# Kernel tuning notes

Measured on AMD Instinct MI355X. Metric: run time of the kernel, lower is better.

Reference implementation:

```python
import jax, jax.numpy as jnp
import numpy as np
from functools import partial

THRESH = 0.6      # objectness sigmoid threshold (forward arg `thresh`)
CASE = 416.0      # input image size (forward arg `case`)
NMS_THRESH = 0.7  # nms(boxes, 0.7, mode='inter')
K_PER_SCALE = 512 # fixed candidate cap per scale (jit-safe stand-in for nonzero())
NEG = -1e9


def _decode_scale(out, t, anchors):
    """out: [N, 3*(5+nc), H, W] -> (boxes [K,9], valid [K]) top-K by objectness."""
    N, C, H, W = out.shape
    v = out.transpose(0, 2, 3, 1).reshape(N, H, W, 3, -1)  # [N,H,W,3,5+nc]
    f = v.dtype
    obj = jax.nn.sigmoid(v[..., 0])                        # cfd = sigmoid(vecs[:,0])
    gy = jnp.arange(H, dtype=f).reshape(1, H, 1, 1)        # idxs[:,1] (row)
    gx = jnp.arange(W, dtype=f).reshape(1, 1, W, 1)        # idxs[:,2] (col)
    gn = jnp.arange(N, dtype=f).reshape(N, 1, 1, 1)
    cx = (gx + v[..., 1]) * t / CASE
    cy = (gy + v[..., 2]) * t / CASE
    w = anchors[:, 0] * jnp.exp(v[..., 3]) / CASE          # anchors[a,0], a = last axis
    h = anchors[:, 1] * jnp.exp(v[..., 4]) / CASE
    cls = jnp.argmax(v[..., 5:], axis=-1).astype(f)
    parts = jnp.broadcast_arrays(gn, cx, cy, w, h, obj, cls, gy + 0 * cx, gx + 0 * cx)
    boxes = jnp.stack(parts, axis=-1).reshape(-1, 9)       # [N*H*W*3, 9]
    mask = (obj > THRESH).reshape(-1)
    score = jnp.where(mask, obj.reshape(-1), NEG)
    k = min(K_PER_SCALE, score.shape[0])
    top_s, top_i = jax.lax.top_k(score, k)
    boxes_k = jnp.take(boxes, top_i, axis=0)
    valid_k = top_s > NEG / 2
    if k < K_PER_SCALE:  # pad to fixed K
        pad = K_PER_SCALE - k
        boxes_k = jnp.concatenate([boxes_k, jnp.zeros((pad, 9), f)], 0)
        valid_k = jnp.concatenate([valid_k, jnp.zeros((pad,), bool)], 0)
    return boxes_k, valid_k


def _nms_inter(boxes, valid):
    """Greedy NMS, iou mode 'inter' = inter_area / min(area_i, area_j)."""
    score = jnp.where(valid, boxes[:, 5], NEG)
    order = jnp.argsort(-score)
    boxes = jnp.take(boxes, order, axis=0)
    valid = jnp.take(valid, order)
    cx, cy, w, h = boxes[:, 1], boxes[:, 2], boxes[:, 3], boxes[:, 4]
    x1, y1, x2, y2 = cx - w / 2, cy - h / 2, cx + w / 2, cy + h / 2
    area = jnp.maximum(x2 - x1, 0) * jnp.maximum(y2 - y1, 0)
    ix = jnp.maximum(0.0, jnp.minimum(x2[:, None], x2[None]) - jnp.maximum(x1[:, None], x1[None]))
    iy = jnp.maximum(0.0, jnp.minimum(y2[:, None], y2[None]) - jnp.maximum(y1[:, None], y1[None]))
    inter = ix * iy
    iou = inter / jnp.maximum(jnp.minimum(area[:, None], area[None]), 1e-9)
    M = boxes.shape[0]
    idx = jnp.arange(M)

    def body(i, keep):
        sup = (iou[i] > NMS_THRESH) & keep[i] & (idx > i)
        return keep & ~sup

    keep = jax.lax.fori_loop(0, M, body, valid)
    return boxes * keep[:, None].astype(boxes.dtype)  # suppressed rows zeroed


def reference(out13, out26, out52, anchors13, anchors26, anchors52):
    b13, v13 = _decode_scale(out13, 32.0, anchors13)
    b26, v26 = _decode_scale(out26, 16.0, anchors26)
    b52, v52 = _decode_scale(out52, 8.0, anchors52)
    boxes = jnp.concatenate([b13, b26, b52], axis=0)   # [3K, 9]
    valid = jnp.concatenate([v13, v26, v52], axis=0)
    return _nms_inter(boxes, valid)


def setup_inputs() -> dict:
    key = jax.random.key(0)
    k = jax.random.split(key, 6)
    N, NC = 32, 80
    C = 3 * (5 + NC)
    return {
        "out13": jax.random.normal(k[0], (N, C, 13, 13), jnp.float32),
        "out26": jax.random.normal(k[1], (N, C, 26, 26), jnp.float32),
        "out52": jax.random.normal(k[2], (N, C, 52, 52), jnp.float32),
        "anchors13": jnp.array([[116, 90], [156, 198], [373, 326]], jnp.float32),
        "anchors26": jnp.array([[30, 61], [62, 45], [59, 119]], jnp.float32),
        "anchors52": jnp.array([[10, 13], [16, 30], [33, 23]], jnp.float32),
    }
```

## Files before the change

kernel.cpp:

```cpp
#include <hip/hip_runtime.h>
#include <stdint.h>

#define KPS 512
#define NBOX 1536
#define NBINS 1024
#define CAP 96

#define S13 16224
#define S26 64896
#define S52 259584
#define TOTCELL 340704

__device__ __forceinline__ uint32_t f2u(float x){ union{float f;uint32_t u;}v; v.f=x; return v.u; }
__device__ __forceinline__ float u2f(uint32_t x){ union{float f;uint32_t u;}v; v.u=x; return v.f; }

__device__ __forceinline__ int binOf(float s){
    int b = (int)((s - 0.6f) * 2560.0f);
    if (b < 0) b = 0;
    if (b > NBINS-1) b = NBINS-1;
    return b;
}

__global__ void k_init(int* hist){
    int id = blockIdx.x*256 + threadIdx.x;
    if (id < 3*NBINS) hist[id] = 0;
}

__global__ void k_score(const float* __restrict__ o13, const float* __restrict__ o26,
                        const float* __restrict__ o52,
                        unsigned long long* __restrict__ bucket, int* __restrict__ hist){
    int id = blockIdx.x*256 + threadIdx.x;
    if (id >= TOTCELL) return;
    int scale, idl, H;
    const float* src;
    if (id < S13)            { scale=0; idl=id;            H=13; src=o13; }
    else if (id < S13+S26)   { scale=1; idl=id-S13;        H=26; src=o26; }
    else                     { scale=2; idl=id-(S13+S26);  H=52; src=o52; }
    int HW = H*H;
    int p  = idl / HW;
    int hw = idl - p*HW;
    int n  = p / 3;
    int a  = p - n*3;
    float x = src[(size_t)(n*255 + a*85)*HW + hw];
    float s = (float)(1.0 / (1.0 + exp(-(double)x)));
    if (s > 0.6f){
        int cidx = (n*HW + hw)*3 + a;
        unsigned long long key = ((unsigned long long)f2u(s) << 20)
            | ((unsigned long long)(2-scale) << 18)
            | (unsigned long long)(262143 - cidx);
        int slot = scale*NBINS + binOf(s);
        int pos = atomicAdd(&hist[slot], 1);
        if (pos < CAP) bucket[(size_t)slot*CAP + pos] = key;
    }
}

__global__ void __launch_bounds__(1024) k_selfin(const int* __restrict__ hist,
                        const unsigned long long* __restrict__ bucket,
                        unsigned long long* __restrict__ sel, int* __restrict__ cnt){
    int s = blockIdx.x, t = threadIdx.x;
    __shared__ int suf[NBINS];
    __shared__ unsigned long long un[640];
    __shared__ int sB;
    int h = hist[s*NBINS + t];
    suf[t] = h; __syncthreads();
    for (int d = 1; d < NBINS; d <<= 1){
        int v = (t + d < NBINS) ? suf[t + d] : 0;
        __syncthreads();
        suf[t] += v;
        __syncthreads();
    }
    int total = suf[0];
    int A = (t < NBINS-1) ? suf[t+1] : 0;
    if (t == 0 && total < KPS) sB = -1;
    if (A < KPS && A + h >= KPS) sB = t;
    __syncthreads();
    int B = sB;
    int Bg = (B < 0) ? 0 : B;
    if (t + Bg < NBINS){
        int b = Bg + t;
        int cb = hist[s*NBINS + b]; if (cb > CAP) cb = CAP;
        int off = (b == NBINS-1) ? 0 : suf[b+1];
        for (int e = 0; e < cb; e++)
            un[off + e] = bucket[(size_t)(s*NBINS + b)*CAP + e];
    }
    __syncthreads();
    int hB = hist[s*NBINS + Bg]; if (hB > CAP) hB = CAP;
    int E = ((Bg == NBINS-1) ? 0 : suf[Bg+1]) + hB;
    int Nsel = (E < KPS) ? E : KPS;
    for (int e = t; e < E; e += 1024){
        unsigned long long k = un[e];
        int rank = 0;
        for (int q = 0; q < E; q++) rank += (un[q] > k) ? 1 : 0;
        if (rank < Nsel) sel[s*KPS + rank] = k;
    }
    if (t < KPS && t >= Nsel) sel[s*KPS + t] = 0ull;
    if (t == 0) cnt[s] = Nsel;
}

__global__ void k_decode_merge(const float* __restrict__ o13, const float* __restrict__ o26,
                         const float* __restrict__ o52,
                         const float* __restrict__ a13, const float* __restrict__ a26,
                         const float* __restrict__ a52,
                         const unsigned long long* __restrict__ sel, const int* __restrict__ cnt,
                         float* __restrict__ sboxes, unsigned long long* __restrict__ vwords){
    __shared__ unsigned long long sk[NBOX];
    int t = threadIdx.x;
    for (int r = t; r < NBOX; r += 256) sk[r] = sel[r];
    __syncthreads();
    int wv = t >> 6, lane = t & 63;
    int b = blockIdx.x*4 + wv;
    unsigned long long key = sk[b];
    int pc = 0;
    for (int q = lane; q < NBOX; q += 64){
        unsigned long long kq = sk[q];
        pc += (kq > key || (kq == key && q < b)) ? 1 : 0;
    }
    #pragma unroll
    for (int off = 32; off; off >>= 1) pc += __shfl_xor(pc, off);
    int rank = pc;
    float* row = sboxes + rank*12;
    if ((key >> 20) == 0ull){
        if (lane < 9) row[lane] = 0.f;
    } else {
        int scale = 2 - (int)((key >> 18) & 3ull);
        int cidx  = 262143 - (int)(key & 0x3FFFFull);
        uint32_t sbits = (uint32_t)(key >> 20);
        const float* src; const float* anch; int H; float tt;
        if (scale == 0){ src=o13; anch=a13; H=13; tt=32.f; }
        else if (scale == 1){ src=o26; anch=a26; H=26; tt=16.f; }
        else { src=o52; anch=a52; H=52; tt=8.f; }
        int HW = H*H;
        int a  = cidx % 3;
        int hw = (cidx/3) % HW;
        int n  = cidx / (3*HW);
        int hh = hw / H;
        int ww = hw - hh*H;
        const float* cellbase = src + (size_t)(n*255 + a*85)*HW + hw;
        float bv = cellbase[(size_t)(5 + lane)*HW];
        int bi = lane;
        if (lane < 16){
            float v2 = cellbase[(size_t)(69 + lane)*HW];
            if (v2 > bv){ bv = v2; bi = 64 + lane; }
        }
        #pragma unroll
        for (int off=32; off; off>>=1){
            float vo = __shfl_xor(bv, off);
            int io = __shfl_xor(bi, off);
            if (vo > bv || (vo == bv && io < bi)){ bv = vo; bi = io; }
        }
        if (lane == 0){
            float v1 = cellbase[(size_t)1*HW];
            float v2 = cellbase[(size_t)2*HW];
            float v3 = cellbase[(size_t)3*HW];
            float v4 = cellbase[(size_t)4*HW];
            float cx = ((float)ww + v1) * tt / 416.0f;
            float cy = ((float)hh + v2) * tt / 416.0f;
            float e3 = (float)exp((double)v3);
            float e4 = (float)exp((double)v4);
            float bw = anch[a*2+0] * e3 / 416.0f;
            float bh = anch[a*2+1] * e4 / 416.0f;
            row[0] = (float)n;  row[1] = cx; row[2] = cy; row[3] = bw; row[4] = bh;
            row[5] = u2f(sbits); row[6] = (float)bi; row[7] = (float)hh; row[8] = (float)ww;
        }
    }
    if (blockIdx.x == 0 && t < 24){
        int nv = cnt[0] + cnt[1] + cnt[2];
        int rem = nv - t*64;
        vwords[t] = rem >= 64 ? ~0ull : (rem <= 0 ? 0ull : ((1ull << rem) - 1ull));
    }
}

__global__ void k_masks(const float* __restrict__ sboxes, unsigned* __restrict__ Tcol,
                        unsigned long long* __restrict__ diagR){
    int i = blockIdx.x;
    int lane = threadIdx.x;
    int gi = i >> 6;
    float cxi = sboxes[i*12+1], cyi = sboxes[i*12+2], wi = sboxes[i*12+3], hi = sboxes[i*12+4];
    float x1i = cxi - wi/2.0f, y1i = cyi - hi/2.0f, x2i = cxi + wi/2.0f, y2i = cyi + hi/2.0f;
    float ari = fmaxf(x2i-x1i, 0.f) * fmaxf(y2i-y1i, 0.f);
    unsigned colbits = 0u;
    for (int c=0; c<24; c++){
        int j = c*64 + lane;
        float cxj = sboxes[j*12+1], cyj = sboxes[j*12+2], wj = sboxes[j*12+3], hj = sboxes[j*12+4];
        float x1j = cxj - wj/2.0f, y1j = cyj - hj/2.0f, x2j = cxj + wj/2.0f, y2j = cyj + hj/2.0f;
        float arj = fmaxf(x2j-x1j, 0.f) * fmaxf(y2j-y1j, 0.f);
        float ix = fmaxf(0.f, fminf(x2i, x2j) - fmaxf(x1i, x1j));
        float iy = fmaxf(0.f, fminf(y2i, y2j) - fmaxf(y1i, y1j));
        float inter = ix * iy;
        float iou = inter / fmaxf(fminf(ari, arj), 1e-9f);
        bool sb = (iou > 0.7f) && (j > i);
        colbits |= sb ? (1u << c) : 0u;
    }
    Tcol[(size_t)i*64 + lane] = colbits;
    unsigned long long rowbits = __ballot(((colbits >> gi) & 1u) != 0u);
    if (lane == 0) diagR[i] = rowbits;
}

__device__ __forceinline__ unsigned long long readlane64(unsigned long long v, int i){
    unsigned lo = (unsigned)__builtin_amdgcn_readlane((int)(unsigned)v, i);
    unsigned hi = (unsigned)__builtin_amdgcn_readlane((int)(unsigned)(v >> 32), i);
    return ((unsigned long long)hi << 32) | (unsigned long long)lo;
}

__global__ void k_nms_out(const float* __restrict__ sboxes, const unsigned long long* __restrict__ vwords,
                          const unsigned long long* __restrict__ diagR, const unsigned* __restrict__ Tcol,
                          float* __restrict__ out){
    __shared__ unsigned long long keepw[24];
    __shared__ unsigned partial[2][4][64];
    int t = threadIdx.x;
    int wv = t >> 6, lane = t & 63;
    unsigned SS = 0u;
    unsigned long long rowR = diagR[lane];
    unsigned long long vcur = vwords[0];
    unsigned rows[16];
    {
        const unsigned* b0 = Tcol + (size_t)(wv*16)*64 + lane;
        #pragma unroll
        for (int i=0;i<16;i++) rows[i] = b0[i*64];
    }
    for (int g = 0; g < 24; g++){
        unsigned long long Rnext = (g < 23) ? diagR[(g+1)*64 + lane] : 0ull;
        unsigned long long vnext = (g < 23) ? vwords[g+1] : 0ull;
        bool live = (((vcur >> lane) & 1ull) != 0ull) && (((SS >> g) & 1u) == 0u);
        unsigned long long pend = __ballot(live);
        unsigned long long Z = __ballot(live && ((rowR & pend) != 0ull));
        unsigned long long kept = pend;
        unsigned long long iter = Z;
        while (iter){
            int i = __ffsll((long long)iter) - 1;
            iter &= iter - 1ull;
            if ((kept >> i) & 1ull){
                unsigned long long sup = readlane64(rowR, i);
                kept &= ~sup;
                iter &= ~sup;
            }
        }
        if (t == 0) keepw[g] = kept;
        unsigned kbits = (unsigned)((kept >> (wv*16)) & 0xFFFFull);
        unsigned acc = 0u;
        #pragma unroll
        for (int i=0;i<16;i++) acc |= (0u - ((kbits >> i) & 1u)) & rows[i];
        if (g < 23){
            const unsigned* nb = Tcol + (size_t)((g+1)*64 + wv*16)*64 + lane;
            #pragma unroll
            for (int i=0;i<16;i++) rows[i] = nb[i*64];
        }
        partial[g & 1][wv][lane] = acc;
        __syncthreads();
        SS |= partial[g & 1][0][lane] | partial[g & 1][1][lane]
            | partial[g & 1][2][lane] | partial[g & 1][3][lane];
        rowR = Rnext; vcur = vnext;
    }
    for (int e=t; e<NBOX*9; e+=256){
        int r = e / 9;
        int c = e - r*9;
        bool kp = ((keepw[r >> 6] >> (r & 63)) & 1ull) != 0ull;
        out[e] = kp ? sboxes[r*12 + c] : 0.f;
    }
}

extern "C" void kernel_launch(void* const* d_in, const int* in_sizes, int n_in,
                              void* d_out, int out_size, void* d_ws, size_t ws_size,
                              hipStream_t stream){
    const float* o13 = (const float*)d_in[0];
    const float* o26 = (const float*)d_in[1];
    const float* o52 = (const float*)d_in[2];
    const float* a13 = (const float*)d_in[3];
    const float* a26 = (const float*)d_in[4];
    const float* a52 = (const float*)d_in[5];
    char* ws = (char*)d_ws;
    unsigned long long* bucket = (unsigned long long*)(ws);
    unsigned* Tcol            = (unsigned*)(ws);
    int* hist                 = (int*)(ws + 2359296);
    int* cnt                  = (int*)(ws + 2371584);
    unsigned long long* sel   = (unsigned long long*)(ws + 2371712);
    float* sboxes             = (float*)(ws + 2384000);
    unsigned long long* vw    = (unsigned long long*)(ws + 2457728);
    unsigned long long* diagR = (unsigned long long*)(ws + 2457984);
    float* out = (float*)d_out;

    k_init        <<<12, 256, 0, stream>>>(hist);
    k_score       <<<(TOTCELL + 255)/256, 256, 0, stream>>>(o13, o26, o52, bucket, hist);
    k_selfin      <<<3, 1024, 0, stream>>>(hist, bucket, sel, cnt);
    k_decode_merge<<<NBOX/4, 256, 0, stream>>>(o13, o26, o52, a13, a26, a52, sel, cnt, sboxes, vw);
    k_masks       <<<NBOX, 64, 0, stream>>>(sboxes, Tcol, diagR);
    k_nms_out     <<<1, 256, 0, stream>>>(sboxes, vw, diagR, Tcol, out);
}
```

Baseline: 230.8 us.

## Fuse all six stages into one cooperative kernel with grid-wide syncs

Replaces the six separate launches (init, score, select, decode/merge, masks, NMS) with one persistent cooperative kernel of 256 blocks × 1024 threads. Stages are separated by grid.sync() barriers, and per-stage shared memory is overlaid in a union. The aim is to remove per-launch overhead and the idle gaps between small dependent kernels. In exchange, several stages now run on fewer, larger blocks: mask building uses 96 blocks instead of 1536, and scoring uses a grid-stride loop. Each grid barrier also has its own cost.

New measurement: 355.5 us. 1.54x slower.

```diff
diff --git a/kernel.cpp b/kernel.cpp
--- a/kernel.cpp
+++ b/kernel.cpp
@@ -1,5 +1,8 @@
 #include <hip/hip_runtime.h>
+#include <hip/hip_cooperative_groups.h>
 #include <stdint.h>
+
+namespace cg = cooperative_groups;
 
 #define KPS 512
 #define NBOX 1536
@@ -21,241 +24,253 @@
     return b;
 }
 
-__global__ void k_init(int* hist){
-    int id = blockIdx.x*256 + threadIdx.x;
-    if (id < 3*NBINS) hist[id] = 0;
-}
-
-__global__ void k_score(const float* __restrict__ o13, const float* __restrict__ o26,
-                        const float* __restrict__ o52,
-                        unsigned long long* __restrict__ bucket, int* __restrict__ hist){
-    int id = blockIdx.x*256 + threadIdx.x;
-    if (id >= TOTCELL) return;
-    int scale, idl, H;
-    const float* src;
-    if (id < S13)            { scale=0; idl=id;            H=13; src=o13; }
-    else if (id < S13+S26)   { scale=1; idl=id-S13;        H=26; src=o26; }
-    else                     { scale=2; idl=id-(S13+S26);  H=52; src=o52; }
-    int HW = H*H;
-    int p  = idl / HW;
-    int hw = idl - p*HW;
-    int n  = p / 3;
-    int a  = p - n*3;
-    float x = src[(size_t)(n*255 + a*85)*HW + hw];
-    float s = (float)(1.0 / (1.0 + exp(-(double)x)));
-    if (s > 0.6f){
-        int cidx = (n*HW + hw)*3 + a;
-        unsigned long long key = ((unsigned long long)f2u(s) << 20)
-            | ((unsigned long long)(2-scale) << 18)
-            | (unsigned long long)(262143 - cidx);
-        int slot = scale*NBINS + binOf(s);
-        int pos = atomicAdd(&hist[slot], 1);
-        if (pos < CAP) bucket[(size_t)slot*CAP + pos] = key;
-    }
-}
-
-__global__ void __launch_bounds__(1024) k_selfin(const int* __restrict__ hist,
-                        const unsigned long long* __restrict__ bucket,
-                        unsigned long long* __restrict__ sel, int* __restrict__ cnt){
-    int s = blockIdx.x, t = threadIdx.x;
-    __shared__ int suf[NBINS];
-    __shared__ unsigned long long un[640];
-    __shared__ int sB;
-    int h = hist[s*NBINS + t];
-    suf[t] = h; __syncthreads();
-    for (int d = 1; d < NBINS; d <<= 1){
-        int v = (t + d < NBINS) ? suf[t + d] : 0;
-        __syncthreads();
-        suf[t] += v;
-        __syncthreads();
-    }
-    int total = suf[0];
-    int A = (t < NBINS-1) ? suf[t+1] : 0;
-    if (t == 0 && total < KPS) sB = -1;
-    if (A < KPS && A + h >= KPS) sB = t;
-    __syncthreads();
-    int B = sB;
-    int Bg = (B < 0) ? 0 : B;
-    if (t + Bg < NBINS){
-        int b = Bg + t;
-        int cb = hist[s*NBINS + b]; if (cb > CAP) cb = CAP;
-        int off = (b == NBINS-1) ? 0 : suf[b+1];
-        for (int e = 0; e < cb; e++)
-            un[off + e] = bucket[(size_t)(s*NBINS + b)*CAP + e];
-    }
-    __syncthreads();
-    int hB = hist[s*NBINS + Bg]; if (hB > CAP) hB = CAP;
-    int E = ((Bg == NBINS-1) ? 0 : suf[Bg+1]) + hB;
-    int Nsel = (E < KPS) ? E : KPS;
-    for (int e = t; e < E; e += 1024){
-        unsigned long long k = un[e];
-        int rank = 0;
-        for (int q = 0; q < E; q++) rank += (un[q] > k) ? 1 : 0;
-        if (rank < Nsel) sel[s*KPS + rank] = k;
-    }
-    if (t < KPS && t >= Nsel) sel[s*KPS + t] = 0ull;
-    if (t == 0) cnt[s] = Nsel;
-}
-
-__global__ void k_decode_merge(const float* __restrict__ o13, const float* __restrict__ o26,
-                         const float* __restrict__ o52,
-                         const float* __restrict__ a13, const float* __restrict__ a26,
-                         const float* __restrict__ a52,
-                         const unsigned long long* __restrict__ sel, const int* __restrict__ cnt,
-                         float* __restrict__ sboxes, unsigned long long* __restrict__ vwords){
-    __shared__ unsigned long long sk[NBOX];
-    int t = threadIdx.x;
-    for (int r = t; r < NBOX; r += 256) sk[r] = sel[r];
-    __syncthreads();
-    int wv = t >> 6, lane = t & 63;
-    int b = blockIdx.x*4 + wv;
-    unsigned long long key = sk[b];
-    int pc = 0;
-    for (int q = lane; q < NBOX; q += 64){
-        unsigned long long kq = sk[q];
-        pc += (kq > key || (kq == key && q < b)) ? 1 : 0;
-    }
-    #pragma unroll
-    for (int off = 32; off; off >>= 1) pc += __shfl_xor(pc, off);
-    int rank = pc;
-    float* row = sboxes + rank*12;
-    if ((key >> 20) == 0ull){
-        if (lane < 9) row[lane] = 0.f;
-    } else {
-        int scale = 2 - (int)((key >> 18) & 3ull);
-        int cidx  = 262143 - (int)(key & 0x3FFFFull);
-        uint32_t sbits = (uint32_t)(key >> 20);
-        const float* src; const float* anch; int H; float tt;
-        if (scale == 0){ src=o13; anch=a13; H=13; tt=32.f; }
-        else if (scale == 1){ src=o26; anch=a26; H=26; tt=16.f; }
-        else { src=o52; anch=a52; H=52; tt=8.f; }
-        int HW = H*H;
-        int a  = cidx % 3;
-        int hw = (cidx/3) % HW;
-        int n  = cidx / (3*HW);
-        int hh = hw / H;
-        int ww = hw - hh*H;
-        const float* cellbase = src + (size_t)(n*255 + a*85)*HW + hw;
-        float bv = cellbase[(size_t)(5 + lane)*HW];
-        int bi = lane;
-        if (lane < 16){
-            float v2 = cellbase[(size_t)(69 + lane)*HW];
-            if (v2 > bv){ bv = v2; bi = 64 + lane; }
-        }
-        #pragma unroll
-        for (int off=32; off; off>>=1){
-            float vo = __shfl_xor(bv, off);
-            int io = __shfl_xor(bi, off);
-            if (vo > bv || (vo == bv && io < bi)){ bv = vo; bi = io; }
-        }
-        if (lane == 0){
-            float v1 = cellbase[(size_t)1*HW];
-            float v2 = cellbase[(size_t)2*HW];
-            float v3 = cellbase[(size_t)3*HW];
-            float v4 = cellbase[(size_t)4*HW];
-            float cx = ((float)ww + v1) * tt / 416.0f;
-            float cy = ((float)hh + v2) * tt / 416.0f;
-            float e3 = (float)exp((double)v3);
-            float e4 = (float)exp((double)v4);
-            float bw = anch[a*2+0] * e3 / 416.0f;
-            float bh = anch[a*2+1] * e4 / 416.0f;
-            row[0] = (float)n;  row[1] = cx; row[2] = cy; row[3] = bw; row[4] = bh;
-            row[5] = u2f(sbits); row[6] = (float)bi; row[7] = (float)hh; row[8] = (float)ww;
-        }
-    }
-    if (blockIdx.x == 0 && t < 24){
-        int nv = cnt[0] + cnt[1] + cnt[2];
-        int rem = nv - t*64;
-        vwords[t] = rem >= 64 ? ~0ull : (rem <= 0 ? 0ull : ((1ull << rem) - 1ull));
-    }
-}
-
-__global__ void k_masks(const float* __restrict__ sboxes, unsigned* __restrict__ Tcol,
-                        unsigned long long* __restrict__ diagR){
-    int i = blockIdx.x;
-    int lane = threadIdx.x;
-    int gi = i >> 6;
-    float cxi = sboxes[i*12+1], cyi = sboxes[i*12+2], wi = sboxes[i*12+3], hi = sboxes[i*12+4];
-    float x1i = cxi - wi/2.0f, y1i = cyi - hi/2.0f, x2i = cxi + wi/2.0f, y2i = cyi + hi/2.0f;
-    float ari = fmaxf(x2i-x1i, 0.f) * fmaxf(y2i-y1i, 0.f);
-    unsigned colbits = 0u;
-    for (int c=0; c<24; c++){
-        int j = c*64 + lane;
-        float cxj = sboxes[j*12+1], cyj = sboxes[j*12+2], wj = sboxes[j*12+3], hj = sboxes[j*12+4];
-        float x1j = cxj - wj/2.0f, y1j = cyj - hj/2.0f, x2j = cxj + wj/2.0f, y2j = cyj + hj/2.0f;
-        float arj = fmaxf(x2j-x1j, 0.f) * fmaxf(y2j-y1j, 0.f);
-        float ix = fmaxf(0.f, fminf(x2i, x2j) - fmaxf(x1i, x1j));
-        float iy = fmaxf(0.f, fminf(y2i, y2j) - fmaxf(y1i, y1j));
-        float inter = ix * iy;
-        float iou = inter / fmaxf(fminf(ari, arj), 1e-9f);
-        bool sb = (iou > 0.7f) && (j > i);
-        colbits |= sb ? (1u << c) : 0u;
-    }
-    Tcol[(size_t)i*64 + lane] = colbits;
-    unsigned long long rowbits = __ballot(((colbits >> gi) & 1u) != 0u);
-    if (lane == 0) diagR[i] = rowbits;
-}
-
 __device__ __forceinline__ unsigned long long readlane64(unsigned long long v, int i){
     unsigned lo = (unsigned)__builtin_amdgcn_readlane((int)(unsigned)v, i);
     unsigned hi = (unsigned)__builtin_amdgcn_readlane((int)(unsigned)(v >> 32), i);
     return ((unsigned long long)hi << 32) | (unsigned long long)lo;
 }
 
-__global__ void k_nms_out(const float* __restrict__ sboxes, const unsigned long long* __restrict__ vwords,
-                          const unsigned long long* __restrict__ diagR, const unsigned* __restrict__ Tcol,
-                          float* __restrict__ out){
-    __shared__ unsigned long long keepw[24];
-    __shared__ unsigned partial[2][4][64];
-    int t = threadIdx.x;
-    int wv = t >> 6, lane = t & 63;
-    unsigned SS = 0u;
-    unsigned long long rowR = diagR[lane];
-    unsigned long long vcur = vwords[0];
-    unsigned rows[16];
-    {
-        const unsigned* b0 = Tcol + (size_t)(wv*16)*64 + lane;
+__global__ void __launch_bounds__(1024) k_mega(
+        const float* __restrict__ o13, const float* __restrict__ o26,
+        const float* __restrict__ o52,
+        const float* __restrict__ a13, const float* __restrict__ a26,
+        const float* __restrict__ a52,
+        unsigned long long* __restrict__ bucket, int* __restrict__ hist,
+        int* __restrict__ cnt, unsigned long long* __restrict__ sel,
+        float* __restrict__ sboxes, unsigned long long* __restrict__ vwords,
+        unsigned long long* __restrict__ diagR, unsigned* __restrict__ Tcol,
+        float* __restrict__ out){
+    cg::grid_group grid = cg::this_grid();
+    int t  = threadIdx.x;
+    int blk = blockIdx.x;
+    int nb  = gridDim.x;
+    int gtid = blk*1024 + t;
+    int nth  = nb*1024;
+
+    __shared__ union {
+        struct { int suf[NBINS]; unsigned long long un[640]; int sB; } sf;
+        unsigned long long sk[NBOX];
+        struct { unsigned long long keepw[24]; unsigned partial[2][4][64]; } nm;
+    } sh;
+
+    for (int id = gtid; id < 3*NBINS; id += nth) hist[id] = 0;
+    grid.sync();
+
+    for (int id = gtid; id < TOTCELL; id += nth){
+        int scale, idl, H;
+        const float* src;
+        if (id < S13)            { scale=0; idl=id;            H=13; src=o13; }
+        else if (id < S13+S26)   { scale=1; idl=id-S13;        H=26; src=o26; }
+        else                     { scale=2; idl=id-(S13+S26);  H=52; src=o52; }
+        int HW = H*H;
+        int p  = idl / HW;
+        int hw = idl - p*HW;
+        int n  = p / 3;
+        int a  = p - n*3;
+        float x = src[(size_t)(n*255 + a*85)*HW + hw];
+        float s = (float)(1.0 / (1.0 + exp(-(double)x)));
+        if (s > 0.6f){
+            int cidx = (n*HW + hw)*3 + a;
+            unsigned long long key = ((unsigned long long)f2u(s) << 20)
+                | ((unsigned long long)(2-scale) << 18)
+                | (unsigned long long)(262143 - cidx);
+            int slot = scale*NBINS + binOf(s);
+            int pos = atomicAdd(&hist[slot], 1);
+            if (pos < CAP) bucket[(size_t)slot*CAP + pos] = key;
+        }
+    }
+    grid.sync();
+
+    if (blk < 3){
+        int s = blk;
+        int h = hist[s*NBINS + t];
+        sh.sf.suf[t] = h; __syncthreads();
+        for (int d = 1; d < NBINS; d <<= 1){
+            int v = (t + d < NBINS) ? sh.sf.suf[t + d] : 0;
+            __syncthreads();
+            sh.sf.suf[t] += v;
+            __syncthreads();
+        }
+        int total = sh.sf.suf[0];
+        int A = (t < NBINS-1) ? sh.sf.suf[t+1] : 0;
+        if (t == 0 && total < KPS) sh.sf.sB = -1;
+        if (A < KPS && A + h >= KPS) sh.sf.sB = t;
+        __syncthreads();
+        int B = sh.sf.sB;
+        int Bg = (B < 0) ? 0 : B;
+        if (t + Bg < NBINS){
+            int b = Bg + t;
+            int cb = hist[s*NBINS + b]; if (cb > CAP) cb = CAP;
+            int off = (b == NBINS-1) ? 0 : sh.sf.suf[b+1];
+            for (int e = 0; e < cb; e++)
+                sh.sf.un[off + e] = bucket[(size_t)(s*NBINS + b)*CAP + e];
+        }
+        __syncthreads();
+        int hB = hist[s*NBINS + Bg]; if (hB > CAP) hB = CAP;
+        int E = ((Bg == NBINS-1) ? 0 : sh.sf.suf[Bg+1]) + hB;
+        int Nsel = (E < KPS) ? E : KPS;
+        for (int e = t; e < E; e += 1024){
+            unsigned long long k = sh.sf.un[e];
+            int rank = 0;
+            for (int q = 0; q < E; q++) rank += (sh.sf.un[q] > k) ? 1 : 0;
+            if (rank < Nsel) sel[s*KPS + rank] = k;
+        }
+        if (t < KPS && t >= Nsel) sel[s*KPS + t] = 0ull;
+        if (t == 0) cnt[s] = Nsel;
+    }
+    grid.sync();
+
+    if (blk < NBOX/16){
+        for (int r = t; r < NBOX; r += 1024) sh.sk[r] = sel[r];
+        __syncthreads();
+        int wv = t >> 6, lane = t & 63;
+        int b = blk*16 + wv;
+        unsigned long long key = sh.sk[b];
+        int pc = 0;
+        for (int q = lane; q < NBOX; q += 64){
+            unsigned long long kq = sh.sk[q];
+            pc += (kq > key || (kq == key && q < b)) ? 1 : 0;
+        }
         #pragma unroll
-        for (int i=0;i<16;i++) rows[i] = b0[i*64];
-    }
-    for (int g = 0; g < 24; g++){
-        unsigned long long Rnext = (g < 23) ? diagR[(g+1)*64 + lane] : 0ull;
-        unsigned long long vnext = (g < 23) ? vwords[g+1] : 0ull;
-        bool live = (((vcur >> lane) & 1ull) != 0ull) && (((SS >> g) & 1u) == 0u);
-        unsigned long long pend = __ballot(live);
-        unsigned long long Z = __ballot(live && ((rowR & pend) != 0ull));
-        unsigned long long kept = pend;
-        unsigned long long iter = Z;
-        while (iter){
-            int i = __ffsll((long long)iter) - 1;
-            iter &= iter - 1ull;
-            if ((kept >> i) & 1ull){
-                unsigned long long sup = readlane64(rowR, i);
-                kept &= ~sup;
-                iter &= ~sup;
-            }
-        }
-        if (t == 0) keepw[g] = kept;
-        unsigned kbits = (unsigned)((kept >> (wv*16)) & 0xFFFFull);
-        unsigned acc = 0u;
-        #pragma unroll
-        for (int i=0;i<16;i++) acc |= (0u - ((kbits >> i) & 1u)) & rows[i];
-        if (g < 23){
-            const unsigned* nb = Tcol + (size_t)((g+1)*64 + wv*16)*64 + lane;
+        for (int off = 32; off; off >>= 1) pc += __shfl_xor(pc, off);
+        int rank = pc;
+        float* row = sboxes + rank*12;
+        if ((key >> 20) == 0ull){
+            if (lane < 9) row[lane] = 0.f;
+        } else {
+            int scale = 2 - (int)((key >> 18) & 3ull);
+            int cidx  = 262143 - (int)(key & 0x3FFFFull);
+            uint32_t sbits = (uint32_t)(key >> 20);
+            const float* src; const float* anch; int H; float tt;
+            if (scale == 0){ src=o13; anch=a13; H=13; tt=32.f; }
+            else if (scale == 1){ src=o26; anch=a26; H=26; tt=16.f; }
+            else { src=o52; anch=a52; H=52; tt=8.f; }
+            int HW = H*H;
+            int a  = cidx % 3;
+            int hw = (cidx/3) % HW;
+            int n  = cidx / (3*HW);
+            int hh = hw / H;
+            int ww = hw - hh*H;
+            const float* cellbase = src + (size_t)(n*255 + a*85)*HW + hw;
+            float bv = cellbase[(size_t)(5 + lane)*HW];
+            int bi = lane;
+            if (lane < 16){
+                float v2 = cellbase[(size_t)(69 + lane)*HW];
+                if (v2 > bv){ bv = v2; bi = 64 + lane; }
+            }
             #pragma unroll
-            for (int i=0;i<16;i++) rows[i] = nb[i*64];
-        }
-        partial[g & 1][wv][lane] = acc;
-        __syncthreads();
-        SS |= partial[g & 1][0][lane] | partial[g & 1][1][lane]
-            | partial[g & 1][2][lane] | partial[g & 1][3][lane];
-        rowR = Rnext; vcur = vnext;
-    }
-    for (int e=t; e<NBOX*9; e+=256){
-        int r = e / 9;
-        int c = e - r*9;
-        bool kp = ((keepw[r >> 6] >> (r & 63)) & 1ull) != 0ull;
-        out[e] = kp ? sboxes[r*12 + c] : 0.f;
+            for (int off=32; off; off>>=1){
+                float vo = __shfl_xor(bv, off);
+                int io = __shfl_xor(bi, off);
+                if (vo > bv || (vo == bv && io < bi)){ bv = vo; bi = io; }
+            }
+            if (lane == 0){
+                float v1 = cellbase[(size_t)1*HW];
+                float v2 = cellbase[(size_t)2*HW];
+                float v3 = cellbase[(size_t)3*HW];
+                float v4 = cellbase[(size_t)4*HW];
+                float cx = ((float)ww + v1) * tt / 416.0f;
+                float cy = ((float)hh + v2) * tt / 416.0f;
+                float e3 = (float)exp((double)v3);
+                float e4 = (float)exp((double)v4);
+                float bw = anch[a*2+0] * e3 / 416.0f;
+                float bh = anch[a*2+1] * e4 / 416.0f;
+                row[0] = (float)n;  row[1] = cx; row[2] = cy; row[3] = bw; row[4] = bh;
+                row[5] = u2f(sbits); row[6] = (float)bi; row[7] = (float)hh; row[8] = (float)ww;
+            }
+        }
+        if (blk == 0 && t < 24){
+            int nv = cnt[0] + cnt[1] + cnt[2];
+            int rem = nv - t*64;
+            vwords[t] = rem >= 64 ? ~0ull : (rem <= 0 ? 0ull : ((1ull << rem) - 1ull));
+        }
+    }
+    grid.sync();
+
+    if (blk < NBOX/16){
+        int wv = t >> 6, lane = t & 63;
+        int i = blk*16 + wv;
+        int gi = i >> 6;
+        float cxi = sboxes[i*12+1], cyi = sboxes[i*12+2], wi = sboxes[i*12+3], hi = sboxes[i*12+4];
+        float x1i = cxi - wi/2.0f, y1i = cyi - hi/2.0f, x2i = cxi + wi/2.0f, y2i = cyi + hi/2.0f;
+        float ari = fmaxf(x2i-x1i, 0.f) * fmaxf(y2i-y1i, 0.f);
+        unsigned colbits = 0u;
+        for (int c=0; c<24; c++){
+            int j = c*64 + lane;
+            float cxj = sboxes[j*12+1], cyj = sboxes[j*12+2], wj = sboxes[j*12+3], hj = sboxes[j*12+4];
+            float x1j = cxj - wj/2.0f, y1j = cyj - hj/2.0f, x2j = cxj + wj/2.0f, y2j = cyj + hj/2.0f;
+            float arj = fmaxf(x2j-x1j, 0.f) * fmaxf(y2j-y1j, 0.f);
+            float ix = fmaxf(0.f, fminf(x2i, x2j) - fmaxf(x1i, x1j));
+            float iy = fmaxf(0.f, fminf(y2i, y2j) - fmaxf(y1i, y1j));
+            float inter = ix * iy;
+            float iou = inter / fmaxf(fminf(ari, arj), 1e-9f);
+            bool sb = (iou > 0.7f) && (j > i);
+            colbits |= sb ? (1u << c) : 0u;
+        }
+        Tcol[(size_t)i*64 + lane] = colbits;
+        unsigned long long rowbits = __ballot(((colbits >> gi) & 1u) != 0u);
+        if (lane == 0) diagR[i] = rowbits;
+    }
+    grid.sync();
+
+    if (blk == 0){
+        int wv = t >> 6, lane = t & 63;
+        bool act = (wv < 4);
+        unsigned SS = 0u;
+        unsigned long long rowR = diagR[lane];
+        unsigned long long vcur = vwords[0];
+        unsigned rows[16];
+        if (act){
+            const unsigned* b0 = Tcol + (size_t)(wv*16)*64 + lane;
+            #pragma unroll
+            for (int i=0;i<16;i++) rows[i] = b0[i*64];
+        }
+        for (int g = 0; g < 24; g++){
+            unsigned long long Rnext = 0ull, vnext = 0ull;
+            if (act && g < 23){
+                Rnext = diagR[(g+1)*64 + lane];
+                vnext = vwords[g+1];
+            }
+            if (act){
+                bool live = (((vcur >> lane) & 1ull) != 0ull) && (((SS >> g) & 1u) == 0u);
+                unsigned long long pend = __ballot(live);
+                unsigned long long Z = __ballot(live && ((rowR & pend) != 0ull));
+                unsigned long long kept = pend;
+                unsigned long long iter = Z;
+                while (iter){
+                    int i = __ffsll((long long)iter) - 1;
+                    iter &= iter - 1ull;
+                    if ((kept >> i) & 1ull){
+                        unsigned long long sup = readlane64(rowR, i);
+                        kept &= ~sup;
+                        iter &= ~sup;
+                    }
+                }
+                if (t == 0) sh.nm.keepw[g] = kept;
+                unsigned kbits = (unsigned)((kept >> (wv*16)) & 0xFFFFull);
+                unsigned acc = 0u;
+                #pragma unroll
+                for (int i=0;i<16;i++) acc |= (0u - ((kbits >> i) & 1u)) & rows[i];
+                if (g < 23){
+                    const unsigned* nbp = Tcol + (size_t)((g+1)*64 + wv*16)*64 + lane;
+                    #pragma unroll
+                    for (int i=0;i<16;i++) rows[i] = nbp[i*64];
+                }
+                sh.nm.partial[g & 1][wv][lane] = acc;
+            }
+            __syncthreads();
+            if (act){
+                SS |= sh.nm.partial[g & 1][0][lane] | sh.nm.partial[g & 1][1][lane]
+                    | sh.nm.partial[g & 1][2][lane] | sh.nm.partial[g & 1][3][lane];
+            }
+            rowR = Rnext; vcur = vnext;
+        }
+        for (int e=t; e<NBOX*9; e+=1024){
+            int r = e / 9;
+            int c = e - r*9;
+            bool kp = ((sh.nm.keepw[r >> 6] >> (r & 63)) & 1ull) != 0ull;
+            out[e] = kp ? sboxes[r*12 + c] : 0.f;
+        }
     }
 }
 
@@ -279,10 +294,11 @@
     unsigned long long* diagR = (unsigned long long*)(ws + 2457984);
     float* out = (float*)d_out;
 
-    k_init        <<<12, 256, 0, stream>>>(hist);
-    k_score       <<<(TOTCELL + 255)/256, 256, 0, stream>>>(o13, o26, o52, bucket, hist);
-    k_selfin      <<<3, 1024, 0, stream>>>(hist, bucket, sel, cnt);
-    k_decode_merge<<<NBOX/4, 256, 0, stream>>>(o13, o26, o52, a13, a26, a52, sel, cnt, sboxes, vw);
-    k_masks       <<<NBOX, 64, 0, stream>>>(sboxes, Tcol, diagR);
-    k_nms_out     <<<1, 256, 0, stream>>>(sboxes, vw, diagR, Tcol, out);
+    void* args[] = { (void*)&o13, (void*)&o26, (void*)&o52,
+                     (void*)&a13, (void*)&a26, (void*)&a52,
+                     (void*)&bucket, (void*)&hist, (void*)&cnt, (void*)&sel,
+                     (void*)&sboxes, (void*)&vw, (void*)&diagR, (void*)&Tcol,
+                     (void*)&out };
+    hipLaunchCooperativeKernel((const void*)k_mega, dim3(256), dim3(1024),
+                               args, 0, stream);
 }
```

## Add sparse suppression-edge list fast path for greedy NMS

Applied to the files above, without the earlier changes.

The mask kernel now also records each nonzero 64-bit suppression word (row index and column chunk) into a compact global edge list using an atomic counter. It stages box coordinates in shared memory and runs 1024-thread blocks. When the edge count fits within the cap, the NMS kernel sorts the edges and runs the greedy pass serially over edges only, skipping the 24-group dense bitmask scan. The original dense path is kept as a fallback when edges overflow. The decode kernel is also relaunched with larger blocks. This aims to cut the serial NMS cost when suppressions are sparse, at the price of atomics and an O(E^2) rank sort.

Measured after the change: 430.3 us. 1.86x slower.

```diff
diff --git a/kernel.cpp b/kernel.cpp
--- a/kernel.cpp
+++ b/kernel.cpp
@@ -5,6 +5,7 @@
 #define NBOX 1536
 #define NBINS 1024
 #define CAP 96
+#define ECAP 512
 
 #define S13 16224
 #define S26 64896
@@ -21,9 +22,16 @@
     return b;
 }
 
-__global__ void k_init(int* hist){
+__device__ __forceinline__ unsigned long long readlane64(unsigned long long v, int i){
+    unsigned lo = (unsigned)__builtin_amdgcn_readlane((int)(unsigned)v, i);
+    unsigned hi = (unsigned)__builtin_amdgcn_readlane((int)(unsigned)(v >> 32), i);
+    return ((unsigned long long)hi << 32) | (unsigned long long)lo;
+}
+
+__global__ void k_init(int* hist, int* cnt){
     int id = blockIdx.x*256 + threadIdx.x;
     if (id < 3*NBINS) hist[id] = 0;
+    if (id < 32) cnt[id] = 0;
 }
 
 __global__ void k_score(const float* __restrict__ o13, const float* __restrict__ o26,
@@ -97,7 +105,8 @@
     if (t == 0) cnt[s] = Nsel;
 }
 
-__global__ void k_decode_merge(const float* __restrict__ o13, const float* __restrict__ o26,
+__global__ void __launch_bounds__(1024) k_decode_merge(
+                         const float* __restrict__ o13, const float* __restrict__ o26,
                          const float* __restrict__ o52,
                          const float* __restrict__ a13, const float* __restrict__ a26,
                          const float* __restrict__ a52,
@@ -105,10 +114,10 @@
                          float* __restrict__ sboxes, unsigned long long* __restrict__ vwords){
     __shared__ unsigned long long sk[NBOX];
     int t = threadIdx.x;
-    for (int r = t; r < NBOX; r += 256) sk[r] = sel[r];
+    for (int r = t; r < NBOX; r += 1024) sk[r] = sel[r];
     __syncthreads();
     int wv = t >> 6, lane = t & 63;
-    int b = blockIdx.x*4 + wv;
+    int b = blockIdx.x*16 + wv;
     unsigned long long key = sk[b];
     int pc = 0;
     for (int q = lane; q < NBOX; q += 64){
@@ -170,18 +179,28 @@
     }
 }
 
-__global__ void k_masks(const float* __restrict__ sboxes, unsigned* __restrict__ Tcol,
-                        unsigned long long* __restrict__ diagR){
-    int i = blockIdx.x;
-    int lane = threadIdx.x;
+__global__ void __launch_bounds__(1024) k_masks(const float* __restrict__ sboxes,
+                        unsigned* __restrict__ Tcol, unsigned long long* __restrict__ diagR,
+                        int* __restrict__ cnt, unsigned* __restrict__ eMeta,
+                        unsigned long long* __restrict__ eMask){
+    __shared__ float gx[NBOX], gy[NBOX], gw[NBOX], gh[NBOX];
+    int t = threadIdx.x;
+    for (int j = t; j < NBOX; j += 1024){
+        gx[j] = sboxes[j*12+1]; gy[j] = sboxes[j*12+2];
+        gw[j] = sboxes[j*12+3]; gh[j] = sboxes[j*12+4];
+    }
+    __syncthreads();
+    int wv = t >> 6, lane = t & 63;
+    int i = blockIdx.x*16 + wv;
     int gi = i >> 6;
-    float cxi = sboxes[i*12+1], cyi = sboxes[i*12+2], wi = sboxes[i*12+3], hi = sboxes[i*12+4];
+    float cxi = gx[i], cyi = gy[i], wi = gw[i], hi = gh[i];
     float x1i = cxi - wi/2.0f, y1i = cyi - hi/2.0f, x2i = cxi + wi/2.0f, y2i = cyi + hi/2.0f;
     float ari = fmaxf(x2i-x1i, 0.f) * fmaxf(y2i-y1i, 0.f);
     unsigned colbits = 0u;
+    unsigned long long dm = 0ull;
     for (int c=0; c<24; c++){
         int j = c*64 + lane;
-        float cxj = sboxes[j*12+1], cyj = sboxes[j*12+2], wj = sboxes[j*12+3], hj = sboxes[j*12+4];
+        float cxj = gx[j], cyj = gy[j], wj = gw[j], hj = gh[j];
         float x1j = cxj - wj/2.0f, y1j = cyj - hj/2.0f, x2j = cxj + wj/2.0f, y2j = cyj + hj/2.0f;
         float arj = fmaxf(x2j-x1j, 0.f) * fmaxf(y2j-y1j, 0.f);
         float ix = fmaxf(0.f, fminf(x2i, x2j) - fmaxf(x1i, x1j));
@@ -190,66 +209,99 @@
         float iou = inter / fmaxf(fminf(ari, arj), 1e-9f);
         bool sb = (iou > 0.7f) && (j > i);
         colbits |= sb ? (1u << c) : 0u;
+        unsigned long long m = __ballot(sb);
+        if (c == gi) dm = m;
+        if (m && lane == 0){
+            int pos = atomicAdd(&cnt[8], 1);
+            if (pos < ECAP){ eMeta[pos] = (unsigned)(i*32 + c); eMask[pos] = m; }
+        }
     }
     Tcol[(size_t)i*64 + lane] = colbits;
-    unsigned long long rowbits = __ballot(((colbits >> gi) & 1u) != 0u);
-    if (lane == 0) diagR[i] = rowbits;
-}
-
-__device__ __forceinline__ unsigned long long readlane64(unsigned long long v, int i){
-    unsigned lo = (unsigned)__builtin_amdgcn_readlane((int)(unsigned)v, i);
-    unsigned hi = (unsigned)__builtin_amdgcn_readlane((int)(unsigned)(v >> 32), i);
-    return ((unsigned long long)hi << 32) | (unsigned long long)lo;
+    if (lane == 0) diagR[i] = dm;
 }
 
 __global__ void k_nms_out(const float* __restrict__ sboxes, const unsigned long long* __restrict__ vwords,
                           const unsigned long long* __restrict__ diagR, const unsigned* __restrict__ Tcol,
+                          const int* __restrict__ cnt, const unsigned* __restrict__ eMeta,
+                          const unsigned long long* __restrict__ eMask,
                           float* __restrict__ out){
     __shared__ unsigned long long keepw[24];
-    __shared__ unsigned partial[2][4][64];
+    __shared__ union {
+        struct { unsigned meta[ECAP]; unsigned meta2[ECAP];
+                 unsigned long long mask[ECAP]; unsigned long long mask2[ECAP]; } eg;
+        struct { unsigned partial[2][4][64]; } od;
+    } sh;
     int t = threadIdx.x;
-    int wv = t >> 6, lane = t & 63;
-    unsigned SS = 0u;
-    unsigned long long rowR = diagR[lane];
-    unsigned long long vcur = vwords[0];
-    unsigned rows[16];
-    {
-        const unsigned* b0 = Tcol + (size_t)(wv*16)*64 + lane;
-        #pragma unroll
-        for (int i=0;i<16;i++) rows[i] = b0[i*64];
-    }
-    for (int g = 0; g < 24; g++){
-        unsigned long long Rnext = (g < 23) ? diagR[(g+1)*64 + lane] : 0ull;
-        unsigned long long vnext = (g < 23) ? vwords[g+1] : 0ull;
-        bool live = (((vcur >> lane) & 1ull) != 0ull) && (((SS >> g) & 1u) == 0u);
-        unsigned long long pend = __ballot(live);
-        unsigned long long Z = __ballot(live && ((rowR & pend) != 0ull));
-        unsigned long long kept = pend;
-        unsigned long long iter = Z;
-        while (iter){
-            int i = __ffsll((long long)iter) - 1;
-            iter &= iter - 1ull;
-            if ((kept >> i) & 1ull){
-                unsigned long long sup = readlane64(rowR, i);
-                kept &= ~sup;
-                iter &= ~sup;
+    int nE = cnt[8];
+    if (nE <= ECAP){
+        for (int e = t; e < nE; e += 256){ sh.eg.meta[e] = eMeta[e]; sh.eg.mask[e] = eMask[e]; }
+        __syncthreads();
+        for (int e = t; e < nE; e += 256){
+            unsigned k = sh.eg.meta[e];
+            int r = 0;
+            for (int q = 0; q < nE; q++) r += (sh.eg.meta[q] < k) ? 1 : 0;
+            sh.eg.meta2[r] = k; sh.eg.mask2[r] = sh.eg.mask[e];
+        }
+        __syncthreads();
+        if (t < 64){
+            int lane = t;
+            unsigned long long kept = (lane < 24) ? vwords[lane] : 0ull;
+            for (int e = 0; e < nE; e++){
+                unsigned meta = __builtin_amdgcn_readfirstlane(sh.eg.meta2[e]);
+                unsigned long long m = sh.eg.mask2[e];
+                int i = (int)(meta >> 5);
+                int c = (int)(meta & 31u);
+                int bit = (int)((readlane64(kept, i >> 6) >> (i & 63)) & 1ull);
+                if (bit && lane == c) kept &= ~m;
             }
-        }
-        if (t == 0) keepw[g] = kept;
-        unsigned kbits = (unsigned)((kept >> (wv*16)) & 0xFFFFull);
-        unsigned acc = 0u;
-        #pragma unroll
-        for (int i=0;i<16;i++) acc |= (0u - ((kbits >> i) & 1u)) & rows[i];
-        if (g < 23){
-            const unsigned* nb = Tcol + (size_t)((g+1)*64 + wv*16)*64 + lane;
+            if (lane < 24) keepw[lane] = kept;
+        }
+        __syncthreads();
+    } else {
+        int wv = t >> 6, lane = t & 63;
+        unsigned SS = 0u;
+        unsigned long long rowR = diagR[lane];
+        unsigned long long vcur = vwords[0];
+        unsigned rows[16];
+        {
+            const unsigned* b0 = Tcol + (size_t)(wv*16)*64 + lane;
             #pragma unroll
-            for (int i=0;i<16;i++) rows[i] = nb[i*64];
-        }
-        partial[g & 1][wv][lane] = acc;
-        __syncthreads();
-        SS |= partial[g & 1][0][lane] | partial[g & 1][1][lane]
-            | partial[g & 1][2][lane] | partial[g & 1][3][lane];
-        rowR = Rnext; vcur = vnext;
+            for (int i=0;i<16;i++) rows[i] = b0[i*64];
+        }
+        for (int g = 0; g < 24; g++){
+            unsigned long long Rnext = (g < 23) ? diagR[(g+1)*64 + lane] : 0ull;
+            unsigned long long vnext = (g < 23) ? vwords[g+1] : 0ull;
+            bool live = (((vcur >> lane) & 1ull) != 0ull) && (((SS >> g) & 1u) == 0u);
+            unsigned long long pend = __ballot(live);
+            unsigned long long Z = __ballot(live && ((rowR & pend) != 0ull));
+            unsigned long long kept = pend;
+            unsigned long long iter = Z;
+            while (iter){
+                int i = __ffsll((long long)iter) - 1;
+                iter &= iter - 1ull;
+                if ((kept >> i) & 1ull){
+                    unsigned long long sup = readlane64(rowR, i);
+                    kept &= ~sup;
+                    iter &= ~sup;
+                }
+            }
+            if (t == 0) keepw[g] = kept;
+            unsigned kbits = (unsigned)((kept >> (wv*16)) & 0xFFFFull);
+            unsigned acc = 0u;
+            #pragma unroll
+            for (int i=0;i<16;i++) acc |= (0u - ((kbits >> i) & 1u)) & rows[i];
+            if (g < 23){
+                const unsigned* nb = Tcol + (size_t)((g+1)*64 + wv*16)*64 + lane;
+                #pragma unroll
+                for (int i=0;i<16;i++) rows[i] = nb[i*64];
+            }
+            sh.od.partial[g & 1][wv][lane] = acc;
+            __syncthreads();
+            SS |= sh.od.partial[g & 1][0][lane] | sh.od.partial[g & 1][1][lane]
+                | sh.od.partial[g & 1][2][lane] | sh.od.partial[g & 1][3][lane];
+            rowR = Rnext; vcur = vnext;
+        }
+        __syncthreads();
     }
     for (int e=t; e<NBOX*9; e+=256){
         int r = e / 9;
@@ -277,12 +329,14 @@
     float* sboxes             = (float*)(ws + 2384000);
     unsigned long long* vw    = (unsigned long long*)(ws + 2457728);
     unsigned long long* diagR = (unsigned long long*)(ws + 2457984);
+    unsigned* eMeta           = (unsigned*)(ws + 2470272);
+    unsigned long long* eMask = (unsigned long long*)(ws + 2472320);
     float* out = (float*)d_out;
 
-    k_init        <<<12, 256, 0, stream>>>(hist);
+    k_init        <<<12, 256, 0, stream>>>(hist, cnt);
     k_score       <<<(TOTCELL + 255)/256, 256, 0, stream>>>(o13, o26, o52, bucket, hist);
     k_selfin      <<<3, 1024, 0, stream>>>(hist, bucket, sel, cnt);
-    k_decode_merge<<<NBOX/4, 256, 0, stream>>>(o13, o26, o52, a13, a26, a52, sel, cnt, sboxes, vw);
-    k_masks       <<<NBOX, 64, 0, stream>>>(sboxes, Tcol, diagR);
-    k_nms_out     <<<1, 256, 0, stream>>>(sboxes, vw, diagR, Tcol, out);
-}
+    k_decode_merge<<<96, 1024, 0, stream>>>(o13, o26, o52, a13, a26, a52, sel, cnt, sboxes, vw);
+    k_masks       <<<96, 1024, 0, stream>>>(sboxes, Tcol, diagR, cnt, eMeta, eMask);
+    k_nms_out     <<<1, 256, 0, stream>>>(sboxes, vw, diagR, Tcol, cnt, eMeta, eMask, out);
+}
```
